# Performance work log

Hardware: AMD Instinct MI355X
Metric: run time of the kernel (lower is better)

## Reference

```python
import jax, jax.numpy as jnp
import numpy as np

B, S, D, H, DK = 2, 2048, 2048, 16, 128
ALIBI_SLOPE = 8.0
NEG = -1e9  # finite stand-in for -inf so gradients stay finite


def setup_inputs() -> dict:
    key = jax.random.key(0)
    ks = jax.random.split(key, 8)
    states = jax.random.normal(ks[0], (B, S, D), jnp.float32)
    # causal ALiBi-style additive bias: -(i-j) for j<=i else very negative
    pos = jnp.arange(S)
    dist = pos[None, :] - pos[:, None]  # j - i
    bias = jnp.where(dist <= 0, dist.astype(jnp.float32), NEG)
    bias_mask = jnp.broadcast_to(bias[None], (B, S, S))
    # per-head scale: exp2(-((h+1)*slope/H))
    head_scale = jnp.exp2(-((jnp.arange(H) + 1.0) * ALIBI_SLOPE / H)).astype(jnp.float32)
    init = lambda k, shp: jax.random.normal(k, shp, jnp.float32) * (shp[-1] ** -0.5)
    return {
        'states': states,
        'bias_mask': bias_mask,
        'head_scale': head_scale,
        'Wq': init(ks[1], (D, D)), 'bq': jnp.zeros((D,), jnp.float32),
        'Wk': init(ks[2], (D, D)), 'bk': jnp.zeros((D,), jnp.float32),
        'Wv': init(ks[3], (D, D)), 'bv': jnp.zeros((D,), jnp.float32),
        'Wg': init(ks[4], (H, D)), 'bg': jnp.zeros((H,), jnp.float32),
        'Wo': init(ks[5], (D, D)), 'bo': jnp.zeros((D,), jnp.float32),
    }


def reference(states, bias_mask, head_scale, Wq, bq, Wk, bk, Wv, bv, Wg, bg, Wo, bo):
    b, s, d = states.shape
    key_scale = DK ** -0.5
    proj = lambda x, W, bias: x @ W.T + bias
    # [b,s,d] -> [b,h,s,dk]
    q = proj(states, Wq, bq).reshape(b, s, H, DK).transpose(0, 2, 1, 3)
    k = proj(states, Wk, bk).reshape(b, s, H, DK).transpose(0, 2, 1, 3)
    v = proj(states, Wv, bv).reshape(b, s, H, DK).transpose(0, 2, 1, 3)
    # additive per-head ALiBi bias: [b,1,s,s] * [1,h,1,1]
    bias = bias_mask[:, None, :, :] * head_scale[None, :, None, None]
    scores = jnp.einsum('bhqd,bhkd->bhqk', q, k) * key_scale + bias
    attn = jax.nn.softmax(scores, axis=-1)
    o = jnp.einsum('bhqk,bhkd->bhqd', attn, v).transpose(0, 2, 1, 3)  # [b,s,h,dk]
    g = jax.nn.sigmoid(proj(states, Wg, bg))  # [b,s,h]
    o = o * g[..., None]
    return proj(o.reshape(b, s, d), Wo, bo)
```

## Files before the change

kernel.cpp:

```cpp
#include <hip/hip_runtime.h>

#define SEQ  2048
#define NROW 4096
#define KDIM 2048
#define NH   16
#define DKH  128
#define CSUB 20.0f
#define LOG2E 1.44269504088896f

typedef unsigned int u32;
typedef unsigned short u16;
typedef __attribute__((ext_vector_type(8))) __bf16 bf16x8;
typedef __attribute__((ext_vector_type(4))) float f32x4;
typedef __attribute__((ext_vector_type(4))) u16 u16x4;

struct alignas(16) U4 { u32 x, y, z, w; };

__device__ __forceinline__ u16 f2bf(float f) {
  u32 u = __builtin_bit_cast(u32, f);
  u32 r = (u + 0x7fffu + ((u >> 16) & 1u)) >> 16;
  return (u16)r;
}
__device__ __forceinline__ u16 f2bf_n(float f) {
  __bf16 h = (__bf16)f;
  return __builtin_bit_cast(u16, h);
}
__device__ __forceinline__ bf16x8 asb(U4 v) { return __builtin_bit_cast(bf16x8, v); }
__device__ __forceinline__ float exp2a(float x) {
  float r;
  asm("v_exp_f32 %0, %1" : "=v"(r) : "v"(x));
  return r;
}

__device__ __forceinline__ void gl2lds16(const u16* g, u16* l) {
  __builtin_amdgcn_global_load_lds(
      (const __attribute__((address_space(1))) void*)g,
      (__attribute__((address_space(3))) void*)l, 16, 0, 0);
}

__global__ __launch_bounds__(256)
void cvtk(const float* __restrict__ src, u16* __restrict__ dst, int n)
{
  const int i = (blockIdx.x * 256 + threadIdx.x) * 4;
  if (i < n) {
    f32x4 v = *(const f32x4*)(src + i);
    u16x4 o;
#pragma unroll
    for (int j = 0; j < 4; ++j) o[j] = f2bf_n(v[j]);
    *(u16x4*)(dst + i) = o;
  }
}

__global__ __launch_bounds__(256)
void cvt3k(const float* __restrict__ s0, const float* __restrict__ s1,
           const float* __restrict__ s2, u16* __restrict__ dst, int n)
{
  const float* s = blockIdx.y == 0 ? s0 : (blockIdx.y == 1 ? s1 : s2);
  u16* d = dst + (size_t)blockIdx.y * n;
  const int i = (blockIdx.x * 256 + threadIdx.x) * 4;
  if (i < n) {
    f32x4 v = *(const f32x4*)(s + i);
    u16x4 o;
#pragma unroll
    for (int j = 0; j < 4; ++j) o[j] = f2bf_n(v[j]);
    *(u16x4*)(d + i) = o;
  }
}

__global__ __launch_bounds__(256)
void gatesg(const float* __restrict__ X, const float* __restrict__ Wg,
            const float* __restrict__ bg, float* __restrict__ G,
            u16* __restrict__ S16)
{
  __shared__ alignas(16) u16 xs16[16 * 2056];
  __shared__ float red[4][16][16];
  const int tid = threadIdx.x;
  const int lane = tid & 63, wave = tid >> 6;
  const int l15 = lane & 15, quad = lane >> 4;
  const int m0 = blockIdx.x * 16;

#pragma unroll
  for (int r = 0; r < 16; ++r) {
    const size_t gofs = (size_t)(m0 + r) * KDIM + tid * 8;
    f32x4 v0 = *(const f32x4*)(X + gofs);
    f32x4 v1 = *(const f32x4*)(X + gofs + 4);
    U4 o;
    o.x = (u32)f2bf_n(v0[0]) | ((u32)f2bf_n(v0[1]) << 16);
    o.y = (u32)f2bf_n(v0[2]) | ((u32)f2bf_n(v0[3]) << 16);
    o.z = (u32)f2bf_n(v1[0]) | ((u32)f2bf_n(v1[1]) << 16);
    o.w = (u32)f2bf_n(v1[2]) | ((u32)f2bf_n(v1[3]) << 16);
    *(U4*)(S16 + gofs) = o;
    *(U4*)(&xs16[r * 2056 + tid * 8]) = o;
  }
  __syncthreads();

  const u16*   Xp = &xs16[l15 * 2056 + wave * 512 + quad * 8];
  const float* Wp = Wg + (size_t)l15 * KDIM + wave * 512 + quad * 8;

  f32x4 acc = {0.f, 0.f, 0.f, 0.f};
#pragma unroll
  for (int kk = 0; kk < 512; kk += 32) {
    U4 a = *(const U4*)(Xp + kk);
    f32x4 w0 = *(const f32x4*)(Wp + kk);
    f32x4 w1 = *(const f32x4*)(Wp + kk + 4);
    U4 bw;
    bw.x = (u32)f2bf_n(w0[0]) | ((u32)f2bf_n(w0[1]) << 16);
    bw.y = (u32)f2bf_n(w0[2]) | ((u32)f2bf_n(w0[3]) << 16);
    bw.z = (u32)f2bf_n(w1[0]) | ((u32)f2bf_n(w1[1]) << 16);
    bw.w = (u32)f2bf_n(w1[2]) | ((u32)f2bf_n(w1[3]) << 16);
    acc = __builtin_amdgcn_mfma_f32_16x16x32_bf16(asb(a), asb(bw), acc, 0, 0, 0);
  }
#pragma unroll
  for (int r = 0; r < 4; ++r) red[wave][quad * 4 + r][l15] = acc[r];
  __syncthreads();
  const int row = tid >> 4, head = tid & 15;
  float s = bg[head];
#pragma unroll
  for (int w = 0; w < 4; ++w) s += red[w][row][head];
  G[(size_t)(m0 + row) * NH + head] = 1.f / (1.f + __expf(-s));
}

__global__ __launch_bounds__(256, 2)
void qkvg(const u16* __restrict__ A, const u16* __restrict__ B,
          const float* __restrict__ bq, const float* __restrict__ bk,
          const float* __restrict__ bv, u16* __restrict__ Qw,
          u16* __restrict__ Kw, u16* __restrict__ Vw)
{
  __shared__ alignas(16) u16 As[128 * 32];
  __shared__ alignas(16) u16 Bs[128 * 32];
  const int tid = threadIdx.x;
  const int lane = tid & 63, wave = tid >> 6;
  const int wm = wave >> 1, wn = wave & 1;
  const int l15 = lane & 15, quad = lane >> 4;
  const int m0 = blockIdx.y * 128, n0 = blockIdx.x * 128;

  f32x4 acc[4][4];
#pragma unroll
  for (int i = 0; i < 4; ++i)
#pragma unroll
    for (int j = 0; j < 4; ++j) acc[i][j] = {0.f, 0.f, 0.f, 0.f};

  const int gr = lane >> 2;
  const int gc = (lane & 3) * 8;

  for (int kk = 0; kk < KDIM; kk += 32) {
#pragma unroll
    for (int it = 0; it < 2; ++it) {
      const int r0 = wave * 32 + it * 16;
      gl2lds16(A + (size_t)(m0 + r0 + gr) * KDIM + kk + gc, As + r0 * 32);
      gl2lds16(B + (size_t)(n0 + r0 + gr) * KDIM + kk + gc, Bs + r0 * 32);
    }
    __syncthreads();
    U4 af[4], bg4[4];
#pragma unroll
    for (int t = 0; t < 4; ++t) {
      af[t]  = *(const U4*)(As + (wm * 64 + t * 16 + l15) * 32 + quad * 8);
      bg4[t] = *(const U4*)(Bs + (wn * 64 + t * 16 + l15) * 32 + quad * 8);
    }
#pragma unroll
    for (int mt = 0; mt < 4; ++mt)
#pragma unroll
      for (int nt = 0; nt < 4; ++nt)
        acc[mt][nt] = __builtin_amdgcn_mfma_f32_16x16x32_bf16(
            asb(af[mt]), asb(bg4[nt]), acc[mt][nt], 0, 0, 0);
    __syncthreads();
  }

  const int seg = n0 >> 11;
  const float* bp = seg == 0 ? bq : (seg == 1 ? bk : bv);
  u16* Cq = seg == 0 ? Qw : Kw;

#pragma unroll
  for (int mt = 0; mt < 4; ++mt) {
    const int rowb = m0 + wm * 64 + mt * 16 + quad * 4;
    const int b = rowb >> 11, srow = rowb & (SEQ - 1);
#pragma unroll
    for (int nt = 0; nt < 4; ++nt) {
      const int col6 = n0 + wn * 64 + nt * 16 + l15;
      const int col = col6 & 2047;
      const int h = col >> 7, dk = col & 127;
      const float bvl = bp[col];
      if (seg == 2) {
        u16x4 pk;
#pragma unroll
        for (int r = 0; r < 4; ++r) pk[r] = f2bf_n(acc[mt][nt][r] + bvl);
        const size_t idx = ((size_t)(b * NH + h) * DKH + dk) * SEQ + srow;
        *(u16x4*)(Vw + idx) = pk;
      } else {
#pragma unroll
        for (int r = 0; r < 4; ++r) {
          const size_t idx = ((size_t)(b * NH + h) * SEQ + (srow + r)) * DKH + dk;
          Cq[idx] = f2bf_n(acc[mt][nt][r] + bvl);
        }
      }
    }
  }
}

__global__ __launch_bounds__(256, 2)
void gemm_bt(const u16* __restrict__ A, const u16* __restrict__ B,
             const float* __restrict__ bias, float* __restrict__ Cf)
{
  __shared__ alignas(16) u16 As[128 * 32];
  __shared__ alignas(16) u16 Bs[128 * 32];
  const int tid = threadIdx.x;
  const int lane = tid & 63, wave = tid >> 6;
  const int wm = wave >> 1, wn = wave & 1;
  const int l15 = lane & 15, quad = lane >> 4;
  const int m0 = blockIdx.y * 128, n0 = blockIdx.x * 128;

  f32x4 acc[4][4];
#pragma unroll
  for (int i = 0; i < 4; ++i)
#pragma unroll
    for (int j = 0; j < 4; ++j) acc[i][j] = {0.f, 0.f, 0.f, 0.f};

  const int gr = lane >> 2;
  const int gc = (lane & 3) * 8;

  for (int kk = 0; kk < KDIM; kk += 32) {
#pragma unroll
    for (int it = 0; it < 2; ++it) {
      const int r0 = wave * 32 + it * 16;
      gl2lds16(A + (size_t)(m0 + r0 + gr) * KDIM + kk + gc, As + r0 * 32);
      gl2lds16(B + (size_t)(n0 + r0 + gr) * KDIM + kk + gc, Bs + r0 * 32);
    }
    __syncthreads();
    U4 af[4], bg4[4];
#pragma unroll
    for (int t = 0; t < 4; ++t) {
      af[t]  = *(const U4*)(As + (wm * 64 + t * 16 + l15) * 32 + quad * 8);
      bg4[t] = *(const U4*)(Bs + (wn * 64 + t * 16 + l15) * 32 + quad * 8);
    }
#pragma unroll
    for (int mt = 0; mt < 4; ++mt)
#pragma unroll
      for (int nt = 0; nt < 4; ++nt)
        acc[mt][nt] = __builtin_amdgcn_mfma_f32_16x16x32_bf16(
            asb(af[mt]), asb(bg4[nt]), acc[mt][nt], 0, 0, 0);
    __syncthreads();
  }

#pragma unroll
  for (int mt = 0; mt < 4; ++mt) {
    const int rowb = m0 + wm * 64 + mt * 16 + quad * 4;
#pragma unroll
    for (int nt = 0; nt < 4; ++nt) {
      const int col = n0 + wn * 64 + nt * 16 + l15;
      const float bv = bias[col];
#pragma unroll
      for (int r = 0; r < 4; ++r)
        Cf[(size_t)(rowb + r) * KDIM + col] = acc[mt][nt][r] + bv;
    }
  }
}

__device__ __forceinline__ void stage_kv(const u16* __restrict__ Kh,
                                         const u16* __restrict__ Vh,
                                         int kk, u16* Ksb, u16* Vsb,
                                         int wave, int lane)
{
  const int rK = lane >> 4, cK = lane & 15;
  const int rV = lane >> 3, cV = lane & 7;
#pragma unroll
  for (int j = 0; j < 4; ++j) {
    const int r0k = wave * 16 + j * 4;
    const int xk = ((j & 1) << 2) | rK;
    gl2lds16(Kh + (size_t)(kk + r0k + rK) * DKH + ((cK ^ xk) * 8),
             Ksb + r0k * 128);
    const int r0v = wave * 32 + j * 8;
    gl2lds16(Vh + (size_t)(r0v + rV) * SEQ + kk + ((cV ^ rV) * 8),
             Vsb + r0v * 64);
  }
}

__global__ __launch_bounds__(256, 2)
void attnk(const u16* __restrict__ Q, const u16* __restrict__ Km,
           const u16* __restrict__ Vt, const float* __restrict__ hsc,
           const float* __restrict__ G, u16* __restrict__ O)
{
  __shared__ alignas(16) u16 Ks[2][64 * 128];
  __shared__ alignas(16) u16 Vs[2][128 * 64];
  __shared__ alignas(16) u16 Ps[4][16 * 72];
  const int tid = threadIdx.x;
  const int lane = tid & 63, wave = tid >> 6;
  const int l15 = lane & 15, quad = lane >> 4;
  const int l7x = l15 & 7;
  const int qt = 31 - blockIdx.y, bh = blockIdx.x;
  const int b = bh >> 4, h = bh & 15;
  const size_t hoff = (size_t)bh * SEQ * DKH;
  const u16* Qh = Q + hoff;
  const u16* Kh = Km + hoff;
  const u16* Vh = Vt + hoff;
  const float hs2 = hsc[h] * LOG2E;
  const float ks2 = 0.08838834764831845f * LOG2E;
  const float csub2 = CSUB * LOG2E;
  const float dstep = 64.0f * hs2;

  const int q0 = qt * 64 + wave * 16;
  const int ntile = qt + 1;

  U4 aq[4];
#pragma unroll
  for (int c = 0; c < 4; ++c)
    aq[c] = *(const U4*)(Qh + (size_t)(q0 + l15) * DKH + c * 32 + quad * 8);

  float base[4][4];
#pragma unroll
  for (int r = 0; r < 4; ++r) {
    const int i = q0 + quad * 4 + r;
#pragma unroll
    for (int nt = 0; nt < 4; ++nt)
      base[r][nt] = (float)(nt * 16 + l15 - i) * hs2 - csub2;
  }

  f32x4 oacc[8];
#pragma unroll
  for (int c = 0; c < 8; ++c) oacc[c] = {0.f, 0.f, 0.f, 0.f};
  float l_lane[4] = {0.f, 0.f, 0.f, 0.f};

  stage_kv(Kh, Vh, 0, Ks[0], Vs[0], wave, lane);

  for (int t = 0; t < ntile; ++t) {
    const int kk = t * 64;
    const int cb = t & 1;
    __syncthreads();
    if (t + 1 < ntile)
      stage_kv(Kh, Vh, kk + 64, Ks[cb ^ 1], Vs[cb ^ 1], wave, lane);

    f32x4 sf[4];
    __builtin_amdgcn_s_setprio(1);
#pragma unroll
    for (int nt = 0; nt < 4; ++nt) {
      f32x4 s = {0.f, 0.f, 0.f, 0.f};
#pragma unroll
      for (int c = 0; c < 4; ++c) {
        U4 bk = *(const U4*)(Ks[cb] + (nt * 16 + l15) * 128 +
                             (((c * 4 + quad) ^ l7x) * 8));
        s = __builtin_amdgcn_mfma_f32_16x16x32_bf16(asb(aq[c]), asb(bk), s, 0, 0, 0);
      }
      sf[nt] = s;
    }
    __builtin_amdgcn_s_setprio(0);

    u16* Pw = &Ps[wave][0];
    const float tf = (float)t;
    if (t + 1 < ntile) {
#pragma unroll
      for (int r = 0; r < 4; ++r) {
#pragma unroll
        for (int nt = 0; nt < 4; ++nt) {
          const float p = exp2a(fmaf(sf[nt][r], ks2, fmaf(tf, dstep, base[r][nt])));
          l_lane[r] += p;
          Pw[(quad * 4 + r) * 72 + nt * 16 + l15] = f2bf_n(p);
        }
      }
    } else {
#pragma unroll
      for (int r = 0; r < 4; ++r) {
        const int i = q0 + quad * 4 + r;
#pragma unroll
        for (int nt = 0; nt < 4; ++nt) {
          const int j = kk + nt * 16 + l15;
          float p = 0.f;
          if (j <= i)
            p = exp2a(fmaf(sf[nt][r], ks2, fmaf(tf, dstep, base[r][nt])));
          l_lane[r] += p;
          Pw[(quad * 4 + r) * 72 + nt * 16 + l15] = f2bf_n(p);
        }
      }
    }
    asm volatile("s_waitcnt lgkmcnt(0)" ::: "memory");
    __builtin_amdgcn_sched_barrier(0);
    U4 pf0 = *(const U4*)(Pw + l15 * 72 + quad * 8);
    U4 pf1 = *(const U4*)(Pw + l15 * 72 + 32 + quad * 8);
    __builtin_amdgcn_s_setprio(1);
#pragma unroll
    for (int c = 0; c < 8; ++c) {
      U4 bv0 = *(const U4*)(Vs[cb] + (c * 16 + l15) * 64 + ((quad ^ l7x) * 8));
      U4 bv1 = *(const U4*)(Vs[cb] + (c * 16 + l15) * 64 + (((quad + 4) ^ l7x) * 8));
      oacc[c] = __builtin_amdgcn_mfma_f32_16x16x32_bf16(asb(pf0), asb(bv0), oacc[c], 0, 0, 0);
      oacc[c] = __builtin_amdgcn_mfma_f32_16x16x32_bf16(asb(pf1), asb(bv1), oacc[c], 0, 0, 0);
    }
    __builtin_amdgcn_s_setprio(0);
  }

  float sc[4];
#pragma unroll
  for (int r = 0; r < 4; ++r) {
#pragma unroll
    for (int d = 1; d < 16; d <<= 1)
      l_lane[r] += __shfl_xor(l_lane[r], d, 64);
    const int i = q0 + quad * 4 + r;
    sc[r] = G[(size_t)(b * SEQ + i) * NH + h] / l_lane[r];
  }

  __syncthreads();
  u16* OL = &Ks[0][0] + wave * 2112;
#pragma unroll
  for (int c = 0; c < 8; ++c)
#pragma unroll
    for (int r = 0; r < 4; ++r)
      OL[(quad * 4 + r) * 132 + c * 16 + l15] = f2bf_n(oacc[c][r] * sc[r]);
  __syncthreads();
#pragma unroll
  for (int o = 0; o < 4; ++o) {
    const int row = o * 4 + quad;
    U4 val = *(const U4*)(OL + row * 132 + l15 * 8);
    *(U4*)(O + ((size_t)(b * SEQ + q0 + row) * NH + h) * DKH + l15 * 8) = val;
  }
}

extern "C" void kernel_launch(void* const* d_in, const int* in_sizes, int n_in,
                              void* d_out, int out_size, void* d_ws, size_t ws_size,
                              hipStream_t stream)
{
  const float* states = (const float*)d_in[0];
  const float* hscale = (const float*)d_in[2];
  const float* Wq = (const float*)d_in[3];
  const float* bq = (const float*)d_in[4];
  const float* Wk = (const float*)d_in[5];
  const float* bk = (const float*)d_in[6];
  const float* Wv = (const float*)d_in[7];
  const float* bv = (const float*)d_in[8];
  const float* Wg = (const float*)d_in[9];
  const float* bg = (const float*)d_in[10];
  const float* Wo = (const float*)d_in[11];
  const float* bo = (const float*)d_in[12];
  float* out = (float*)d_out;

  char* ws = (char*)d_ws;
  const size_t MB = 1024 * 1024;
  u16* S16  = (u16*)(ws);
  u16* Qw   = (u16*)(ws + 16 * MB);
  u16* Kw   = (u16*)(ws + 32 * MB);
  u16* Vw   = (u16*)(ws + 48 * MB);
  u16* W16  = (u16*)(ws + 64 * MB);
  u16* Ow   = (u16*)(ws + 64 * MB);
  u16* Wo16 = (u16*)(ws);
  float* Gw = out;

  const int NW = KDIM * KDIM;
  dim3 blk(256);

  gatesg<<<dim3(NROW / 16), blk, 0, stream>>>(states, Wg, bg, Gw, S16);
  cvt3k<<<dim3(NW / 1024, 3), blk, 0, stream>>>(Wq, Wk, Wv, W16, NW);
  qkvg<<<dim3(48, 32), blk, 0, stream>>>(S16, W16, bq, bk, bv, Qw, Kw, Vw);
  cvtk<<<dim3(NW / 1024), blk, 0, stream>>>(Wo, Wo16, NW);
  attnk<<<dim3(32, 32), blk, 0, stream>>>(Qw, Kw, Vw, hscale, Gw, Ow);
  gemm_bt<<<dim3(16, 32), blk, 0, stream>>>(Ow, Wo16, bo, out);
}
```

Measured before the change: 413.9 us.

## Fuse weight bf16 conversions into gate and attention kernels; XCD-swizzle GEMM blocks

Removes the standalone conversion launches for Wq/Wk/Wv and Wo. The Wqkv conversion now runs as a tail of the gate kernel and the Wo conversion as a prologue of the attention kernel, saving launch gaps and letting the conversion overlap other work. The QKV and output GEMMs also remap block indices so consecutive tiles land on the same XCD, to improve L2 reuse. The cost is extra per-block memory traffic inside the attention and gate kernels, which may delay their main work.

```diff
diff --git a/kernel.cpp b/kernel.cpp
--- a/kernel.cpp
+++ b/kernel.cpp
@@ -16,11 +16,6 @@
 
 struct alignas(16) U4 { u32 x, y, z, w; };
 
-__device__ __forceinline__ u16 f2bf(float f) {
-  u32 u = __builtin_bit_cast(u32, f);
-  u32 r = (u + 0x7fffu + ((u >> 16) & 1u)) >> 16;
-  return (u16)r;
-}
 __device__ __forceinline__ u16 f2bf_n(float f) {
   __bf16 h = (__bf16)f;
   return __builtin_bit_cast(u16, h);
@@ -39,38 +34,11 @@
 }
 
 __global__ __launch_bounds__(256)
-void cvtk(const float* __restrict__ src, u16* __restrict__ dst, int n)
-{
-  const int i = (blockIdx.x * 256 + threadIdx.x) * 4;
-  if (i < n) {
-    f32x4 v = *(const f32x4*)(src + i);
-    u16x4 o;
-#pragma unroll
-    for (int j = 0; j < 4; ++j) o[j] = f2bf_n(v[j]);
-    *(u16x4*)(dst + i) = o;
-  }
-}
-
-__global__ __launch_bounds__(256)
-void cvt3k(const float* __restrict__ s0, const float* __restrict__ s1,
-           const float* __restrict__ s2, u16* __restrict__ dst, int n)
-{
-  const float* s = blockIdx.y == 0 ? s0 : (blockIdx.y == 1 ? s1 : s2);
-  u16* d = dst + (size_t)blockIdx.y * n;
-  const int i = (blockIdx.x * 256 + threadIdx.x) * 4;
-  if (i < n) {
-    f32x4 v = *(const f32x4*)(s + i);
-    u16x4 o;
-#pragma unroll
-    for (int j = 0; j < 4; ++j) o[j] = f2bf_n(v[j]);
-    *(u16x4*)(d + i) = o;
-  }
-}
-
-__global__ __launch_bounds__(256)
 void gatesg(const float* __restrict__ X, const float* __restrict__ Wg,
             const float* __restrict__ bg, float* __restrict__ G,
-            u16* __restrict__ S16)
+            u16* __restrict__ S16,
+            const float* __restrict__ Wq, const float* __restrict__ Wk,
+            const float* __restrict__ Wv, u16* __restrict__ W16)
 {
   __shared__ alignas(16) u16 xs16[16 * 2056];
   __shared__ float red[4][16][16];
@@ -118,6 +86,23 @@
 #pragma unroll
   for (int w = 0; w < 4; ++w) s += red[w][row][head];
   G[(size_t)(m0 + row) * NH + head] = 1.f / (1.f + __expf(-s));
+
+  const int NW = KDIM * KDIM;
+  const int base = (blockIdx.x * 256 + tid) * 4;
+  const int stride = 256 * 256 * 4;
+#pragma unroll
+  for (int w = 0; w < 3; ++w) {
+    const float* src = w == 0 ? Wq : (w == 1 ? Wk : Wv);
+    u16* dst = W16 + (size_t)w * NW;
+    for (int sidx = 0; sidx < 16; ++sidx) {
+      const int i = base + sidx * stride;
+      f32x4 v = *(const f32x4*)(src + i);
+      u16x4 o;
+#pragma unroll
+      for (int j = 0; j < 4; ++j) o[j] = f2bf_n(v[j]);
+      *(u16x4*)(dst + i) = o;
+    }
+  }
 }
 
 __global__ __launch_bounds__(256, 2)
@@ -132,7 +117,9 @@
   const int lane = tid & 63, wave = tid >> 6;
   const int wm = wave >> 1, wn = wave & 1;
   const int l15 = lane & 15, quad = lane >> 4;
-  const int m0 = blockIdx.y * 128, n0 = blockIdx.x * 128;
+  const int f = blockIdx.y * 48 + blockIdx.x;
+  const int virt = (f & 7) * 192 + (f >> 3);
+  const int m0 = (virt / 48) * 128, n0 = (virt % 48) * 128;
 
   f32x4 acc[4][4];
 #pragma unroll
@@ -207,7 +194,9 @@
   const int lane = tid & 63, wave = tid >> 6;
   const int wm = wave >> 1, wn = wave & 1;
   const int l15 = lane & 15, quad = lane >> 4;
-  const int m0 = blockIdx.y * 128, n0 = blockIdx.x * 128;
+  const int f = blockIdx.y * 16 + blockIdx.x;
+  const int virt = (f & 7) * 64 + (f >> 3);
+  const int m0 = (virt / 16) * 128, n0 = (virt % 16) * 128;
 
   f32x4 acc[4][4];
 #pragma unroll
@@ -277,7 +266,8 @@
 __global__ __launch_bounds__(256, 2)
 void attnk(const u16* __restrict__ Q, const u16* __restrict__ Km,
            const u16* __restrict__ Vt, const float* __restrict__ hsc,
-           const float* __restrict__ G, u16* __restrict__ O)
+           const float* __restrict__ G, u16* __restrict__ O,
+           const float* __restrict__ WoF, u16* __restrict__ Wo16)
 {
   __shared__ alignas(16) u16 Ks[2][64 * 128];
   __shared__ alignas(16) u16 Vs[2][128 * 64];
@@ -288,6 +278,21 @@
   const int l7x = l15 & 7;
   const int qt = 31 - blockIdx.y, bh = blockIdx.x;
   const int b = bh >> 4, h = bh & 15;
+
+  {
+    const int fb = blockIdx.y * 32 + bh;
+    const int base = fb * 4096 + tid * 4;
+#pragma unroll
+    for (int s = 0; s < 4; ++s) {
+      const int i = base + s * 1024;
+      f32x4 v = *(const f32x4*)(WoF + i);
+      u16x4 o;
+#pragma unroll
+      for (int j = 0; j < 4; ++j) o[j] = f2bf_n(v[j]);
+      *(u16x4*)(Wo16 + i) = o;
+    }
+  }
+
   const size_t hoff = (size_t)bh * SEQ * DKH;
   const u16* Qh = Q + hoff;
   const u16* Kh = Km + hoff;
@@ -440,13 +445,11 @@
   u16* Wo16 = (u16*)(ws);
   float* Gw = out;
 
-  const int NW = KDIM * KDIM;
   dim3 blk(256);
 
-  gatesg<<<dim3(NROW / 16), blk, 0, stream>>>(states, Wg, bg, Gw, S16);
-  cvt3k<<<dim3(NW / 1024, 3), blk, 0, stream>>>(Wq, Wk, Wv, W16, NW);
+  gatesg<<<dim3(NROW / 16), blk, 0, stream>>>(states, Wg, bg, Gw, S16,
+                                              Wq, Wk, Wv, W16);
   qkvg<<<dim3(48, 32), blk, 0, stream>>>(S16, W16, bq, bk, bv, Qw, Kw, Vw);
-  cvtk<<<dim3(NW / 1024), blk, 0, stream>>>(Wo, Wo16, NW);
-  attnk<<<dim3(32, 32), blk, 0, stream>>>(Qw, Kw, Vw, hscale, Gw, Ow);
+  attnk<<<dim3(32, 32), blk, 0, stream>>>(Qw, Kw, Vw, hscale, Gw, Ow, Wo, Wo16);
   gemm_bt<<<dim3(16, 32), blk, 0, stream>>>(Ow, Wo16, bo, out);
 }
```

Result: no change. 418.5 us (+1.1%).
